# Performance work log

Measured on AMD Instinct MI355X. Metric: run time of the kernel, lower is better.

## Reference

```python
import jax, jax.numpy as jnp
import numpy as np

EPS = 1e-12  # torch F.normalize eps

def _l2norm(v, axis):
    n = jnp.sqrt(jnp.sum(v * v, axis=axis, keepdims=True))
    return v / jnp.maximum(n, EPS)

def setup_inputs() -> dict:
    key = jax.random.key(0)
    k1, k2, k3 = jax.random.split(key, 3)
    B, M, D, K = 32, 2048, 1024, 64
    init_sc = 1.0 / np.sqrt(D)
    x = jax.random.normal(k1, (B, M, D), dtype=jnp.float32)
    W = init_sc * jax.random.normal(k2, (K, D), dtype=jnp.float32)          # fc1.weight
    centroids = init_sc * jax.random.normal(k3, (K, D), dtype=jnp.float32)  # self.centeroids
    return {"x": x, "W": W, "centroids": centroids}

def reference(x, W, centroids):
    # x: [B, M, D] frame features; W, centroids: [K, D]
    x = _l2norm(x, axis=-1)                                   # per-frame L2 normalize
    logits = jnp.einsum('bmd,kd->bmk', x, W)                  # fc1 (no bias)
    a = jax.nn.softmax(logits, axis=-1)                       # soft assignment [B, M, K]
    # vlad[b,k,:] = sum_m a[b,m,k] * (x[b,m,:] - centroids[k,:])
    #            = (A^T X)[b,k,:] - (sum_m a[b,m,k]) * centroids[k,:]
    vlad = jnp.einsum('bmk,bmd->bkd', a, x) - a.sum(axis=1)[..., None] * centroids
    vlad = _l2norm(vlad, axis=-1)                             # intra-normalization per cluster
    v = vlad.reshape(vlad.shape[0], -1)                       # [B, K*D]
    return _l2norm(v, axis=-1)                                # global L2 normalize
```

## Files before the change

### kernel.cpp

```cpp
#include <hip/hip_runtime.h>
#include <math.h>


#define NB 32
#define NM 2048
#define ND 1024
#define NK 64

typedef float f32x4 __attribute__((ext_vector_type(4)));
typedef short s16x4 __attribute__((ext_vector_type(4)));
typedef short s16x8 __attribute__((ext_vector_type(8)));

static constexpr float EPS_ = 1e-12f;

__device__ __forceinline__ short f2bf(float f) {
    union { float f; unsigned u; } v; v.f = f;
    unsigned r = v.u + 0x7fffu + ((v.u >> 16) & 1u);
    return (short)(r >> 16);
}

__device__ __forceinline__ void gload16(const void* g, void* l) {
    __builtin_amdgcn_global_load_lds(
        (const __attribute__((address_space(1))) void*)g,
        (__attribute__((address_space(3))) void*)l, 16, 0, 0);
}

__global__ __launch_bounds__(256) void nv1_logits_softmax(
    const float* __restrict__ x, const float* __restrict__ W,
    short* __restrict__ aT, short* __restrict__ xbT, float* __restrict__ asum)
{
    const int b = blockIdx.y, mt = blockIdx.x;
    const int tid  = threadIdx.x;
    const int w    = tid >> 6, lane = tid & 63, g = lane >> 4, c = lane & 15;
    const int wm   = w >> 1, wk = w & 1;

    __shared__ union {
        struct { short Xs[64][72]; short Ws[64][72]; } st;
        float Ls[64][68];
    } sm;
    __shared__ float red[64][16];
    __shared__ float inv_l[64];
    __shared__ float asum_l[64];

    f32x4 acc[2][2] = {};
    float sq[4] = {0.f, 0.f, 0.f, 0.f};

    const int sr = tid >> 4;
    const int sc = tid & 15;
    const float* xb = x + ((size_t)b * NM + (size_t)mt * 64) * ND;

    for (int d0 = 0; d0 < ND; d0 += 64) {
        __syncthreads();
        #pragma unroll
        for (int i = 0; i < 4; ++i) {
            const int r = sr + 16 * i;
            const float4 xv = *(const float4*)(xb + (size_t)r * ND + d0 + sc * 4);
            const float4 wv = *(const float4*)(W  + (size_t)r * ND + d0 + sc * 4);
            sq[i] += xv.x*xv.x + xv.y*xv.y + xv.z*xv.z + xv.w*xv.w;
            s16x4 xh, wh;
            xh[0]=f2bf(xv.x); xh[1]=f2bf(xv.y); xh[2]=f2bf(xv.z); xh[3]=f2bf(xv.w);
            wh[0]=f2bf(wv.x); wh[1]=f2bf(wv.y); wh[2]=f2bf(wv.z); wh[3]=f2bf(wv.w);
            *(s16x4*)&sm.st.Xs[r][sc * 4] = xh;
            *(s16x4*)&sm.st.Ws[r][sc * 4] = wh;
            const int dg   = d0 + sc * 4;
            const int dt_  = dg >> 7;
            const int dblk = (dg >> 4) & 7;
            const size_t gp = (((size_t)(b * 32 + mt) * 8 + dt_) << 13)
                            + (size_t)((dblk * 16 + (r >> 2)) * 64 + (r & 3) * 16 + (dg & 15));
            *(s16x4*)(xbT + gp) = xh;
        }
        __syncthreads();
        #pragma unroll
        for (int s = 0; s < 2; ++s) {
            s16x8 af[2], bf[2];
            #pragma unroll
            for (int f = 0; f < 2; ++f) {
                af[f] = *(const s16x8*)&sm.st.Xs[wm*32 + f*16 + c][s*32 + g*8];
                bf[f] = *(const s16x8*)&sm.st.Ws[wk*32 + f*16 + c][s*32 + g*8];
            }
            #pragma unroll
            for (int fm = 0; fm < 2; ++fm)
                #pragma unroll
                for (int fk = 0; fk < 2; ++fk)
                    acc[fm][fk] = __builtin_amdgcn_mfma_f32_16x16x32_bf16(
                        af[fm], bf[fk], acc[fm][fk], 0, 0, 0);
        }
    }
    __syncthreads();
    #pragma unroll
    for (int i = 0; i < 4; ++i) red[sr + 16*i][sc] = sq[i];
    #pragma unroll
    for (int fm = 0; fm < 2; ++fm)
        #pragma unroll
        for (int fk = 0; fk < 2; ++fk)
            #pragma unroll
            for (int r = 0; r < 4; ++r)
                sm.Ls[wm*32 + fm*16 + g*4 + r][wk*32 + fk*16 + c] = acc[fm][fk][r];
    __syncthreads();
    if (tid < 64) {
        float s = 0.f;
        #pragma unroll
        for (int i = 0; i < 16; ++i) s += red[tid][i];
        inv_l[tid]  = 1.f / fmaxf(sqrtf(s), EPS_);
        asum_l[tid] = 0.f;
    }
    __syncthreads();

    const int row = tid >> 2, q = tid & 3;
    const float iv = inv_l[row];
    float e[16];
    float mx = -3.0e38f;
    #pragma unroll
    for (int j = 0; j < 16; ++j) { e[j] = sm.Ls[row][q*16 + j] * iv; mx = fmaxf(mx, e[j]); }
    mx = fmaxf(mx, __shfl_xor(mx, 1, 64));
    mx = fmaxf(mx, __shfl_xor(mx, 2, 64));
    float smv = 0.f;
    #pragma unroll
    for (int j = 0; j < 16; ++j) { e[j] = __expf(e[j] - mx); smv += e[j]; }
    smv += __shfl_xor(smv, 1, 64);
    smv += __shfl_xor(smv, 2, 64);
    const float rs = 1.f / smv;
    #pragma unroll
    for (int j = 0; j < 16; ++j) e[j] *= rs;

    alignas(16) short av[16];
    #pragma unroll
    for (int j = 0; j < 16; ++j) av[j] = f2bf(e[j] * iv);
    {
        const size_t base = ((size_t)(b * 32 + mt)) * 4096
                          + (size_t)(q * 16 + (row >> 2)) * 64 + (size_t)(row & 3) * 16;
        *(int4*)(aT + base)     = *(int4*)&av[0];
        *(int4*)(aT + base + 8) = *(int4*)&av[8];
    }
    #pragma unroll
    for (int msk = 4; msk <= 32; msk <<= 1)
        #pragma unroll
        for (int j = 0; j < 16; ++j) e[j] += __shfl_xor(e[j], msk, 64);
    if ((tid & 60) == 0)
        #pragma unroll
        for (int j = 0; j < 16; ++j) atomicAdd(&asum_l[q*16 + j], e[j]);
    __syncthreads();
    if (tid < 64) atomicAdd(asum + b * 64 + tid, asum_l[tid]);
}

__global__ __launch_bounds__(512) void nv2_vlad(
    const short* __restrict__ xbT, const short* __restrict__ aT,
    const float* __restrict__ asum, const float* __restrict__ cent,
    float* __restrict__ out, float* __restrict__ rowsq)
{
    const int b = blockIdx.y, dt = blockIdx.x;
    const int tid  = threadIdx.x;
    const int w    = tid >> 6, lane = tid & 63, g = lane >> 4, c = lane & 15;
    const int wk   = w >> 2, wd = w & 3;

    __shared__ short Xl[3][8192];
    __shared__ short Al[3][4096];
    __shared__ float rsq_l[64];

    if (tid < 64) rsq_l[tid] = 0.f;

    f32x4 acc[2][2] = {};

    auto STAGE = [&](int mc, int p) {
        const short* xs  = xbT + (((size_t)(b * 32 + mc) * 8 + dt) << 13);
        const short* as_ = aT  + ((size_t)(b * 32 + mc) << 12);
        gload16(xs  + w * 1024 + lane * 8,       &Xl[p][w * 1024]);
        gload16(xs  + w * 1024 + 512 + lane * 8, &Xl[p][w * 1024 + 512]);
        gload16(as_ + w * 512 + lane * 8,        &Al[p][w * 512]);
    };

    auto COMPUTE = [&](int p) {
        const uint32_t ab_ = (uint32_t)(uintptr_t)&Al[p][0];
        const uint32_t xb_ = (uint32_t)(uintptr_t)&Xl[p][0];
        s16x4 A[2][2][2], B[2][2][2];
        #pragma unroll
        for (int f = 0; f < 2; ++f)
            #pragma unroll
            for (int s = 0; s < 2; ++s)
                #pragma unroll
                for (int r = 0; r < 2; ++r) {
                    const uint32_t srow = (uint32_t)(s*8 + g*2 + r);
                    const uint32_t aoff = ab_ + (((uint32_t)(wk*2 + f)*16u + srow)*128u) + (uint32_t)c*8u;
                    const uint32_t boff = xb_ + (((uint32_t)(wd*2 + f)*16u + srow)*128u) + (uint32_t)c*8u;
                    asm volatile("ds_read_b64_tr_b16 %0, %1" : "=v"(A[f][s][r]) : "v"(aoff));
                    asm volatile("ds_read_b64_tr_b16 %0, %1" : "=v"(B[f][s][r]) : "v"(boff));
                }
        asm volatile("s_waitcnt lgkmcnt(0)" ::: "memory");
        __builtin_amdgcn_sched_barrier(0);
        #pragma unroll
        for (int s = 0; s < 2; ++s)
            #pragma unroll
            for (int fk = 0; fk < 2; ++fk) {
                const s16x8 af = __builtin_shufflevector(A[fk][s][0], A[fk][s][1], 0,1,2,3,4,5,6,7);
                #pragma unroll
                for (int fd = 0; fd < 2; ++fd) {
                    const s16x8 bf = __builtin_shufflevector(B[fd][s][0], B[fd][s][1], 0,1,2,3,4,5,6,7);
                    acc[fk][fd] = __builtin_amdgcn_mfma_f32_16x16x32_bf16(af, bf, acc[fk][fd], 0, 0, 0);
                }
            }
    };

    STAGE(0, 0);
    STAGE(1, 1);
    for (int mc = 0; mc < 32; ++mc) {
        if (mc < 31) asm volatile("s_waitcnt vmcnt(3)" ::: "memory");
        else         asm volatile("s_waitcnt vmcnt(0)" ::: "memory");
        __builtin_amdgcn_s_barrier();
        if (mc + 2 < 32) STAGE(mc + 2, (mc + 2) % 3);
        COMPUTE(mc % 3);
    }

    const float* cb = cent + (size_t)dt * 128;
    #pragma unroll
    for (int fk = 0; fk < 2; ++fk)
        #pragma unroll
        for (int r = 0; r < 4; ++r) {
            const int k = wk*32 + fk*16 + g*4 + r;
            const float as = asum[b * 64 + k];
            float s2 = 0.f;
            #pragma unroll
            for (int fd = 0; fd < 2; ++fd) {
                const int d = wd*32 + fd*16 + c;
                const float v = acc[fk][fd][r] - as * cb[(size_t)k * ND + d];
                out[((size_t)b * 64 + k) * ND + (size_t)dt * 128 + d] = v;
                s2 += v * v;
            }
            s2 += __shfl_xor(s2, 1, 64);
            s2 += __shfl_xor(s2, 2, 64);
            s2 += __shfl_xor(s2, 4, 64);
            s2 += __shfl_xor(s2, 8, 64);
            if (c == 0) atomicAdd(&rsq_l[k], s2);
        }
    __syncthreads();
    if (tid < 64) atomicAdd(rowsq + b * 64 + tid, rsq_l[tid]);
}

__global__ __launch_bounds__(256) void nv3_norm(
    float* __restrict__ out, const float* __restrict__ rowsq)
{
    const int b = blockIdx.y, ck = blockIdx.x;
    const int tid = threadIdx.x;
    __shared__ float rinv[64];
    __shared__ float gred[64];
    __shared__ float ginv_s;
    if (tid < 64) {
        const float rs = rowsq[b * NK + tid];
        const float n  = fmaxf(sqrtf(rs), EPS_);
        rinv[tid] = 1.f / n;
        gred[tid] = (rs / n) / n;
    }
    __syncthreads();
    if (tid == 0) {
        float s = 0.f;
        for (int k = 0; k < 64; ++k) s += gred[k];
        ginv_s = 1.f / fmaxf(sqrtf(s), EPS_);
    }
    __syncthreads();
    const float gi = ginv_s;
    float* ob = out + (size_t)b * (NK * ND);
    #pragma unroll
    for (int it = 0; it < 4; ++it) {
        const int idx = ck * 4096 + it * 1024 + tid * 4;
        const float sc = rinv[idx >> 10] * gi;
        float4 v = *(float4*)(ob + idx);
        v.x *= sc; v.y *= sc; v.z *= sc; v.w *= sc;
        *(float4*)(ob + idx) = v;
    }
}

extern "C" void kernel_launch(void* const* d_in, const int* in_sizes, int n_in,
                              void* d_out, int out_size, void* d_ws, size_t ws_size,
                              hipStream_t stream)
{
    const float* x    = (const float*)d_in[0];
    const float* W    = (const float*)d_in[1];
    const float* cent = (const float*)d_in[2];
    float* out = (float*)d_out;

    short* aT    = (short*)d_ws;
    short* xbT   = (short*)((char*)d_ws + (size_t)NB * NM * NK * 2);
    float* asum  = (float*)((char*)d_ws + (size_t)NB * NM * NK * 2 + (size_t)NB * NM * ND * 2);
    float* rowsq = asum + NB * NK;

    hipMemsetAsync(asum, 0, 2 * NB * NK * sizeof(float), stream);

    nv1_logits_softmax<<<dim3(NM / 64, NB), 256, 0, stream>>>(x, W, aT, xbT, asum);
    nv2_vlad<<<dim3(ND / 128, NB), 512, 0, stream>>>(xbT, aT, asum, cent, out, rowsq);
    nv3_norm<<<dim3(16, NB), 256, 0, stream>>>(out, rowsq);
}
```

Baseline: 433.9 us.

## Widen staging loads, use packed bf16 convert, deepen pipeline, drop atomics and memset

The logits kernel now has each thread load 8 consecutive floats and convert them with the hardware packed bf16 instruction, so each store to shared memory and to the xbT buffer is 16 bytes wide. Global atomics for the cluster sums and row squared norms are replaced by per-block partial buffers that the next kernel reduces, which removes the memset launch. The VLAD kernel's LDS pipeline goes from 3 to 4 stages, raising shared memory use to hide more load latency. The change in bf16 rounding path could slightly alter numerics for NaN or edge values.

```diff
diff --git a/kernel.cpp b/kernel.cpp
--- a/kernel.cpp
+++ b/kernel.cpp
@@ -18,6 +18,16 @@
     unsigned r = v.u + 0x7fffu + ((v.u >> 16) & 1u);
     return (short)(r >> 16);
 }
+__device__ __forceinline__ int cvt2(float lo, float hi) {
+    int r; asm("v_cvt_pk_bf16_f32 %0, %1, %2" : "=v"(r) : "v"(lo), "v"(hi));
+    return r;
+}
+__device__ __forceinline__ int4 cvt8(const float4 a, const float4 b) {
+    int4 r;
+    r.x = cvt2(a.x, a.y); r.y = cvt2(a.z, a.w);
+    r.z = cvt2(b.x, b.y); r.w = cvt2(b.z, b.w);
+    return r;
+}
 
 __device__ __forceinline__ void gload16(const void* g, void* l) {
     __builtin_amdgcn_global_load_lds(
@@ -27,7 +37,7 @@
 
 __global__ __launch_bounds__(256) void nv1_logits_softmax(
     const float* __restrict__ x, const float* __restrict__ W,
-    short* __restrict__ aT, short* __restrict__ xbT, float* __restrict__ asum)
+    short* __restrict__ aT, short* __restrict__ xbT, float* __restrict__ asum_part)
 {
     const int b = blockIdx.y, mt = blockIdx.x;
     const int tid  = threadIdx.x;
@@ -38,36 +48,37 @@
         struct { short Xs[64][72]; short Ws[64][72]; } st;
         float Ls[64][68];
     } sm;
-    __shared__ float red[64][16];
+    __shared__ float red[64][8];
     __shared__ float inv_l[64];
     __shared__ float asum_l[64];
 
     f32x4 acc[2][2] = {};
-    float sq[4] = {0.f, 0.f, 0.f, 0.f};
-
-    const int sr = tid >> 4;
-    const int sc = tid & 15;
+    float sq[2] = {0.f, 0.f};
+
+    const int r0  = tid >> 3;
+    const int dg8 = (tid & 7) << 3;
     const float* xb = x + ((size_t)b * NM + (size_t)mt * 64) * ND;
+    const size_t tb = ((size_t)(b * 32 + mt) * 8) << 13;
 
     for (int d0 = 0; d0 < ND; d0 += 64) {
         __syncthreads();
-        #pragma unroll
-        for (int i = 0; i < 4; ++i) {
-            const int r = sr + 16 * i;
-            const float4 xv = *(const float4*)(xb + (size_t)r * ND + d0 + sc * 4);
-            const float4 wv = *(const float4*)(W  + (size_t)r * ND + d0 + sc * 4);
-            sq[i] += xv.x*xv.x + xv.y*xv.y + xv.z*xv.z + xv.w*xv.w;
-            s16x4 xh, wh;
-            xh[0]=f2bf(xv.x); xh[1]=f2bf(xv.y); xh[2]=f2bf(xv.z); xh[3]=f2bf(xv.w);
-            wh[0]=f2bf(wv.x); wh[1]=f2bf(wv.y); wh[2]=f2bf(wv.z); wh[3]=f2bf(wv.w);
-            *(s16x4*)&sm.st.Xs[r][sc * 4] = xh;
-            *(s16x4*)&sm.st.Ws[r][sc * 4] = wh;
-            const int dg   = d0 + sc * 4;
-            const int dt_  = dg >> 7;
-            const int dblk = (dg >> 4) & 7;
-            const size_t gp = (((size_t)(b * 32 + mt) * 8 + dt_) << 13)
-                            + (size_t)((dblk * 16 + (r >> 2)) * 64 + (r & 3) * 16 + (dg & 15));
-            *(s16x4*)(xbT + gp) = xh;
+        const int d    = d0 + dg8;
+        const int dblk = (d >> 4) & 7;
+        const size_t gpb = tb + ((size_t)(d >> 7) << 13) + (size_t)dblk * 1024 + (size_t)(d & 15);
+        #pragma unroll
+        for (int j = 0; j < 2; ++j) {
+            const int r = r0 + 32 * j;
+            const float4 xv0 = *(const float4*)(xb + (size_t)r * ND + d);
+            const float4 xv1 = *(const float4*)(xb + (size_t)r * ND + d + 4);
+            const float4 wv0 = *(const float4*)(W  + (size_t)r * ND + d);
+            const float4 wv1 = *(const float4*)(W  + (size_t)r * ND + d + 4);
+            sq[j] += xv0.x*xv0.x + xv0.y*xv0.y + xv0.z*xv0.z + xv0.w*xv0.w
+                   + xv1.x*xv1.x + xv1.y*xv1.y + xv1.z*xv1.z + xv1.w*xv1.w;
+            const int4 px = cvt8(xv0, xv1);
+            const int4 pw = cvt8(wv0, wv1);
+            *(int4*)&sm.st.Xs[r][dg8] = px;
+            *(int4*)&sm.st.Ws[r][dg8] = pw;
+            *(int4*)(xbT + gpb + (size_t)(r >> 2) * 64 + (size_t)(r & 3) * 16) = px;
         }
         __syncthreads();
         #pragma unroll
@@ -87,8 +98,8 @@
         }
     }
     __syncthreads();
-    #pragma unroll
-    for (int i = 0; i < 4; ++i) red[sr + 16*i][sc] = sq[i];
+    red[r0][tid & 7]      = sq[0];
+    red[r0 + 32][tid & 7] = sq[1];
     #pragma unroll
     for (int fm = 0; fm < 2; ++fm)
         #pragma unroll
@@ -100,7 +111,7 @@
     if (tid < 64) {
         float s = 0.f;
         #pragma unroll
-        for (int i = 0; i < 16; ++i) s += red[tid][i];
+        for (int i = 0; i < 8; ++i) s += red[tid][i];
         inv_l[tid]  = 1.f / fmaxf(sqrtf(s), EPS_);
         asum_l[tid] = 0.f;
     }
@@ -123,14 +134,16 @@
     #pragma unroll
     for (int j = 0; j < 16; ++j) e[j] *= rs;
 
-    alignas(16) short av[16];
-    #pragma unroll
-    for (int j = 0; j < 16; ++j) av[j] = f2bf(e[j] * iv);
     {
+        int4 p0, p1;
+        p0.x = cvt2(e[0]*iv,  e[1]*iv);  p0.y = cvt2(e[2]*iv,  e[3]*iv);
+        p0.z = cvt2(e[4]*iv,  e[5]*iv);  p0.w = cvt2(e[6]*iv,  e[7]*iv);
+        p1.x = cvt2(e[8]*iv,  e[9]*iv);  p1.y = cvt2(e[10]*iv, e[11]*iv);
+        p1.z = cvt2(e[12]*iv, e[13]*iv); p1.w = cvt2(e[14]*iv, e[15]*iv);
         const size_t base = ((size_t)(b * 32 + mt)) * 4096
                           + (size_t)(q * 16 + (row >> 2)) * 64 + (size_t)(row & 3) * 16;
-        *(int4*)(aT + base)     = *(int4*)&av[0];
-        *(int4*)(aT + base + 8) = *(int4*)&av[8];
+        *(int4*)(aT + base)     = p0;
+        *(int4*)(aT + base + 8) = p1;
     }
     #pragma unroll
     for (int msk = 4; msk <= 32; msk <<= 1)
@@ -140,24 +153,32 @@
         #pragma unroll
         for (int j = 0; j < 16; ++j) atomicAdd(&asum_l[q*16 + j], e[j]);
     __syncthreads();
-    if (tid < 64) atomicAdd(asum + b * 64 + tid, asum_l[tid]);
+    if (tid < 64) asum_part[(size_t)(b * 32 + mt) * 64 + tid] = asum_l[tid];
 }
 
 __global__ __launch_bounds__(512) void nv2_vlad(
     const short* __restrict__ xbT, const short* __restrict__ aT,
-    const float* __restrict__ asum, const float* __restrict__ cent,
-    float* __restrict__ out, float* __restrict__ rowsq)
+    const float* __restrict__ asum_part, const float* __restrict__ cent,
+    float* __restrict__ out, float* __restrict__ rowsq_part)
 {
     const int b = blockIdx.y, dt = blockIdx.x;
     const int tid  = threadIdx.x;
     const int w    = tid >> 6, lane = tid & 63, g = lane >> 4, c = lane & 15;
     const int wk   = w >> 2, wd = w & 3;
 
-    __shared__ short Xl[3][8192];
-    __shared__ short Al[3][4096];
+    __shared__ short Xl[4][8192];
+    __shared__ short Al[4][4096];
     __shared__ float rsq_l[64];
-
-    if (tid < 64) rsq_l[tid] = 0.f;
+    __shared__ float asum_s[64];
+
+    if (tid < 64) {
+        rsq_l[tid] = 0.f;
+        float s = 0.f;
+        const float* ap = asum_part + (size_t)b * 2048 + tid;
+        #pragma unroll
+        for (int j = 0; j < 32; ++j) s += ap[j * 64];
+        asum_s[tid] = s;
+    }
 
     f32x4 acc[2][2] = {};
 
@@ -202,12 +223,14 @@
 
     STAGE(0, 0);
     STAGE(1, 1);
+    STAGE(2, 2);
     for (int mc = 0; mc < 32; ++mc) {
-        if (mc < 31) asm volatile("s_waitcnt vmcnt(3)" ::: "memory");
-        else         asm volatile("s_waitcnt vmcnt(0)" ::: "memory");
+        if (mc < 30)      asm volatile("s_waitcnt vmcnt(6)" ::: "memory");
+        else if (mc == 30) asm volatile("s_waitcnt vmcnt(3)" ::: "memory");
+        else              asm volatile("s_waitcnt vmcnt(0)" ::: "memory");
         __builtin_amdgcn_s_barrier();
-        if (mc + 2 < 32) STAGE(mc + 2, (mc + 2) % 3);
-        COMPUTE(mc % 3);
+        if (mc + 3 < 32) STAGE(mc + 3, (mc + 3) & 3);
+        COMPUTE(mc & 3);
     }
 
     const float* cb = cent + (size_t)dt * 128;
@@ -216,7 +239,7 @@
         #pragma unroll
         for (int r = 0; r < 4; ++r) {
             const int k = wk*32 + fk*16 + g*4 + r;
-            const float as = asum[b * 64 + k];
+            const float as = asum_s[k];
             float s2 = 0.f;
             #pragma unroll
             for (int fd = 0; fd < 2; ++fd) {
@@ -232,11 +255,11 @@
             if (c == 0) atomicAdd(&rsq_l[k], s2);
         }
     __syncthreads();
-    if (tid < 64) atomicAdd(rowsq + b * 64 + tid, rsq_l[tid]);
+    if (tid < 64) rowsq_part[(size_t)(b * 8 + dt) * 64 + tid] = rsq_l[tid];
 }
 
 __global__ __launch_bounds__(256) void nv3_norm(
-    float* __restrict__ out, const float* __restrict__ rowsq)
+    float* __restrict__ out, const float* __restrict__ rowsq_part)
 {
     const int b = blockIdx.y, ck = blockIdx.x;
     const int tid = threadIdx.x;
@@ -244,8 +267,11 @@
     __shared__ float gred[64];
     __shared__ float ginv_s;
     if (tid < 64) {
-        const float rs = rowsq[b * NK + tid];
-        const float n  = fmaxf(sqrtf(rs), EPS_);
+        float rs = 0.f;
+        const float* rp = rowsq_part + (size_t)b * 512 + tid;
+        #pragma unroll
+        for (int j = 0; j < 8; ++j) rs += rp[j * 64];
+        const float n = fmaxf(sqrtf(rs), EPS_);
         rinv[tid] = 1.f / n;
         gred[tid] = (rs / n) / n;
     }
@@ -277,14 +303,12 @@
     const float* cent = (const float*)d_in[2];
     float* out = (float*)d_out;
 
-    short* aT    = (short*)d_ws;
-    short* xbT   = (short*)((char*)d_ws + (size_t)NB * NM * NK * 2);
-    float* asum  = (float*)((char*)d_ws + (size_t)NB * NM * NK * 2 + (size_t)NB * NM * ND * 2);
-    float* rowsq = asum + NB * NK;
-
-    hipMemsetAsync(asum, 0, 2 * NB * NK * sizeof(float), stream);
-
-    nv1_logits_softmax<<<dim3(NM / 64, NB), 256, 0, stream>>>(x, W, aT, xbT, asum);
-    nv2_vlad<<<dim3(ND / 128, NB), 512, 0, stream>>>(xbT, aT, asum, cent, out, rowsq);
-    nv3_norm<<<dim3(16, NB), 256, 0, stream>>>(out, rowsq);
-}
+    short* aT         = (short*)d_ws;
+    short* xbT        = (short*)((char*)d_ws + (size_t)NB * NM * NK * 2);
+    float* asum_part  = (float*)((char*)d_ws + (size_t)NB * NM * NK * 2 + (size_t)NB * NM * ND * 2);
+    float* rowsq_part = asum_part + NB * 32 * 64;
+
+    nv1_logits_softmax<<<dim3(NM / 64, NB), 256, 0, stream>>>(x, W, aT, xbT, asum_part);
+    nv2_vlad<<<dim3(ND / 128, NB), 512, 0, stream>>>(xbT, aT, asum_part, cent, out, rowsq_part);
+    nv3_norm<<<dim3(16, NB), 256, 0, stream>>>(out, rowsq_part);
+}
```

Result: no change. 428.8 us (-1.2%).
